# Kernel tuning notes

Hardware: AMD Instinct MI355X
Metric: run time of the kernel (lower is better)

## Reference

```python
import jax, jax.numpy as jnp
import numpy as np

IN_F = 4096
OUT_F = 4096
B, S = 4, 2048


def _rand_ortho(n, seed):
    # stand-in for method.rand_ortho_butterfly: a random orthogonal matrix
    rng = np.random.default_rng(seed)
    q, _ = np.linalg.qr(rng.standard_normal((n, n)).astype(np.float64))
    return jnp.asarray(q, dtype=jnp.float32)


def setup_inputs() -> dict:
    key = jax.random.key(0)
    k_x, k_q, k_s, k_b = jax.random.split(key, 4)
    x = jax.random.normal(k_x, (B, S, IN_F), dtype=jnp.float32)
    qweight = jax.random.randint(k_q, (IN_F, OUT_F), 0, 16, dtype=jnp.int32)
    scale = jnp.float32(1.0)
    # per-column rescale; keep away from zero to avoid blowup in division
    scaleWH = jax.random.uniform(k_s, (IN_F,), dtype=jnp.float32, minval=0.5, maxval=1.5)
    bias = jax.random.normal(k_b, (OUT_F,), dtype=jnp.float32)
    U = _rand_ortho(OUT_F, 51934)   # w.shape[0] = outfeatures
    V = _rand_ortho(IN_F, 51935)    # w.shape[1] = infeatures
    return {"x": x, "qweight": qweight, "scale": scale, "scaleWH": scaleWH,
            "bias": bias, "U": U, "V": V}


def reference(x, qweight, scale, scaleWH, bias, U, V):
    # dequantize: qweight[in,out] -> w[out,in] in [-1,1] * scale
    w = qweight.T.astype(jnp.float32) / 15.0 * 2.0 - 1.0  # [out, in]
    w = w * scale
    # incoherence transform: U^T @ w @ V (dense orthogonal 'butterfly')
    w = U.T @ w @ V                                        # [out, in]
    # diagonal rescaling over the input dimension
    w = w / scaleWH[None, :]
    # F.linear(x, w, bias) = x @ w.T + bias
    return jnp.einsum('bsi,oi->bso', x, w) + bias
```

## Files before the change

kernel.cpp:

```cpp
#include <hip/hip_runtime.h>


#define KT128 128

typedef __attribute__((ext_vector_type(4))) float f32x4;
typedef __attribute__((ext_vector_type(4))) int   i32x4;
typedef __attribute__((ext_vector_type(8))) short s16x8;
typedef __attribute__((ext_vector_type(4))) short s16x4;

__device__ __forceinline__ unsigned short f2bf(float f){
  unsigned u = __builtin_bit_cast(unsigned, f);
  u += 0x7FFFu + ((u >> 16) & 1u);
  return (unsigned short)(u >> 16);
}
__device__ __forceinline__ float bf2f(unsigned short h){
  unsigned u = ((unsigned)h) << 16;
  return __builtin_bit_cast(float, u);
}
__device__ __forceinline__ void splitbf(float v, short &hi, short &lo){
  unsigned short h = f2bf(v);
  float r = v - bf2f(h);
  hi = (short)h;
  lo = (short)f2bf(r);
}

__device__ __forceinline__ void stage16(const short* g, short* l){
  __builtin_amdgcn_global_load_lds((const __attribute__((address_space(1))) void*)g,
                                   (__attribute__((address_space(3))) void*)l,
                                   16, 0, 0);
}

template<int MODE>
__global__ __launch_bounds__(256)
void pack_rows_kernel(const void* __restrict__ srcv,
                      const float* __restrict__ scale_p,
                      short* __restrict__ Oh, short* __restrict__ Ol)
{
  __shared__ float lds[128][33];
  const int kt = blockIdx.x;
  const int mt = blockIdx.y;
  const int t  = threadIdx.x;
  float dq_a = 1.0f, dq_b = 0.0f;
  if (MODE == 1){ float sc = scale_p[0]; dq_a = sc * (2.0f/15.0f); dq_b = -sc; }
  const int rrow = t >> 3;
  const int c4   = t & 7;
  #pragma unroll
  for (int rr = 0; rr < 4; ++rr){
    const int row = rr*32 + rrow;
    const size_t soff = ((size_t)(mt*128 + row))*4096 + (size_t)kt*32 + c4*4;
    if (MODE == 0){
      const f32x4 v = *(const f32x4*)((const float*)srcv + soff);
      #pragma unroll
      for (int j=0;j<4;++j) lds[row][c4*4+j] = v[j];
    } else {
      const i32x4 v = *(const i32x4*)((const int*)srcv + soff);
      #pragma unroll
      for (int j=0;j<4;++j) lds[row][c4*4+j] = (float)v[j]*dq_a + dq_b;
    }
  }
  __syncthreads();
  #pragma unroll
  for (int rnd=0; rnd<2; ++rnd){
    const int cc = rnd*256 + t;
    const int kgp = cc >> 7, mr = cc & 127;
    s16x8 h8, l8;
    #pragma unroll
    for (int j=0;j<8;++j){
      short h,l; splitbf(lds[mr][kgp*8+j], h, l);
      h8[j]=h; l8[j]=l;
    }
    const size_t chunk = ((((size_t)mt*KT128 + kt)*4 + kgp)*128 + mr)*8;
    *(s16x8*)(Oh + chunk) = h8;
    *(s16x8*)(Ol + chunk) = l8;
  }
}

__global__ __launch_bounds__(256)
void pack_cols_kernel(const float* __restrict__ src,
                      short* __restrict__ Oh, short* __restrict__ Ol)
{
  __shared__ float lds[32][132];
  const int kt = blockIdx.x;
  const int xt = blockIdx.y;
  const int t  = threadIdx.x;
  const int o4 = t >> 5;
  const int c4 = t & 31;
  #pragma unroll
  for (int rr=0; rr<4; ++rr){
    const int o = rr*8 + o4;
    const size_t soff = ((size_t)(kt*32 + o))*4096 + (size_t)xt*128 + c4*4;
    const f32x4 v = *(const f32x4*)(src + soff);
    *(f32x4*)&lds[o][c4*4] = v;
  }
  __syncthreads();
  #pragma unroll
  for (int rnd=0; rnd<2; ++rnd){
    const int cc = rnd*256 + t;
    const int kgp = cc >> 7, xr = cc & 127;
    s16x8 h8, l8;
    #pragma unroll
    for (int j=0;j<8;++j){
      short h,l; splitbf(lds[kgp*8+j][xr], h, l);
      h8[j]=h; l8[j]=l;
    }
    const size_t chunk = ((((size_t)xt*KT128 + kt)*4 + kgp)*128 + xr)*8;
    *(s16x8*)(Oh + chunk) = h8;
    *(s16x8*)(Ol + chunk) = l8;
  }
}

template<int EPI>
__global__ __launch_bounds__(256, 2)
void gemm_bf16x3(const short* __restrict__ Ah, const short* __restrict__ Al,
                 const short* __restrict__ Bh, const short* __restrict__ Bl,
                 float* __restrict__ outF, const float* __restrict__ bias,
                 short* __restrict__ Oh, short* __restrict__ Ol,
                 const float* __restrict__ rowScale)
{
  __shared__ short ls[16384];
  short* lsAh = ls;
  short* lsAl = ls + 4096;
  short* lsBh = ls + 8192;
  short* lsBl = ls + 12288;

  const int t    = threadIdx.x;
  const int lane = t & 63, wave = t >> 6;
  const int wr   = wave >> 1, wc = wave & 1;
  const int nt   = blockIdx.x, mt = blockIdx.y;
  const int lr   = lane & 15, kg = lane >> 4;

  f32x4 acc[4][4];
  #pragma unroll
  for (int i=0;i<4;++i)
    #pragma unroll
    for (int j=0;j<4;++j)
      acc[i][j] = f32x4{0.f,0.f,0.f,0.f};

  const short* bAh = Ah + ((size_t)mt*KT128)*4096;
  const short* bAl = Al + ((size_t)mt*KT128)*4096;
  const short* bBh = Bh + ((size_t)nt*KT128)*4096;
  const short* bBl = Bl + ((size_t)nt*KT128)*4096;

  for (int kt = 0; kt < KT128; ++kt){
    const size_t to = (size_t)kt*4096;
    #pragma unroll
    for (int rnd=0; rnd<2; ++rnd){
      const int lo_ = rnd*2048 + wave*512;
      const int go  = lo_ + lane*8;
      stage16(bAh + to + go, lsAh + lo_);
      stage16(bAl + to + go, lsAl + lo_);
      stage16(bBh + to + go, lsBh + lo_);
      stage16(bBl + to + go, lsBl + lo_);
    }
    __syncthreads();

    s16x8 a_h[4], a_l[4];
    #pragma unroll
    for (int fm=0; fm<4; ++fm){
      const int row = wr*64 + fm*16 + lr;
      a_h[fm] = *(const s16x8*)(lsAh + (kg*128 + row)*8);
      a_l[fm] = *(const s16x8*)(lsAl + (kg*128 + row)*8);
    }
    #pragma unroll
    for (int fn=0; fn<4; ++fn){
      const int col = wc*64 + fn*16 + lr;
      const s16x8 b_h = *(const s16x8*)(lsBh + (kg*128 + col)*8);
      const s16x8 b_l = *(const s16x8*)(lsBl + (kg*128 + col)*8);
      #pragma unroll
      for (int fm=0; fm<4; ++fm){
        f32x4 c = acc[fm][fn];
        c = __builtin_amdgcn_mfma_f32_16x16x32_bf16(a_h[fm], b_h, c, 0,0,0);
        c = __builtin_amdgcn_mfma_f32_16x16x32_bf16(a_h[fm], b_l, c, 0,0,0);
        c = __builtin_amdgcn_mfma_f32_16x16x32_bf16(a_l[fm], b_h, c, 0,0,0);
        acc[fm][fn] = c;
      }
    }
    __syncthreads();
  }

  const int r0 = (lane >> 4) * 4;
  if (EPI == 1){
    #pragma unroll
    for (int fm=0; fm<4; ++fm){
      const int gm = mt*128 + wr*64 + fm*16 + r0;
      #pragma unroll
      for (int fn=0; fn<4; ++fn){
        const int gn = nt*128 + wc*64 + fn*16 + lr;
        const float b = bias[gn];
        #pragma unroll
        for (int reg=0; reg<4; ++reg)
          outF[(size_t)(gm+reg)*4096 + gn] = acc[fm][fn][reg] + b;
      }
    }
  } else {
    #pragma unroll
    for (int fm=0; fm<4; ++fm){
      const int rowBase = mt*128 + wr*64 + fm*16 + r0;
      float rs[4];
      #pragma unroll
      for (int reg=0; reg<4; ++reg)
        rs[reg] = rowScale ? (1.0f / rowScale[rowBase+reg]) : 1.0f;
      const int ktp = rowBase >> 5;
      const int kgp = (rowBase >> 3) & 3;
      const int rp  = rowBase & 7;
      #pragma unroll
      for (int fn=0; fn<4; ++fn){
        const int nr = wc*64 + fn*16 + lr;
        const size_t chunk = ((((size_t)nt*KT128 + ktp)*4 + kgp)*128 + nr)*8 + rp;
        s16x4 h4, l4;
        #pragma unroll
        for (int reg=0; reg<4; ++reg){
          short h,l; splitbf(acc[fm][fn][reg]*rs[reg], h, l);
          h4[reg]=h; l4[reg]=l;
        }
        *(s16x4*)(Oh + chunk) = h4;
        *(s16x4*)(Ol + chunk) = l4;
      }
    }
  }
}

extern "C" void kernel_launch(void* const* d_in, const int* in_sizes, int n_in,
                              void* d_out, int out_size, void* d_ws, size_t ws_size,
                              hipStream_t stream)
{
  const float* x      = (const float*)d_in[0];
  const int*   qw     = (const int*)  d_in[1];
  const float* scale  = (const float*)d_in[2];
  const float* sWH    = (const float*)d_in[3];
  const float* bias   = (const float*)d_in[4];
  const float* U      = (const float*)d_in[5];
  const float* V      = (const float*)d_in[6];
  float* out = (float*)d_out;

  const size_t SZW = (size_t)4096*4096;
  if (ws_size < 6*SZW*sizeof(short)) return;

  short* ws  = (short*)d_ws;
  short* Dh  = ws;
  short* Dl  = ws + SZW;
  short* Uh  = ws + 2*SZW;
  short* Ul  = ws + 3*SZW;
  short* A1h = ws + 4*SZW;
  short* A1l = ws + 5*SZW;
  short* Xh  = ws + 4*SZW;
  short* Xl  = ws;

  dim3 blk(256);

  pack_rows_kernel<1><<<dim3(128,32), blk, 0, stream>>>((const void*)qw, scale, Dh, Dl);
  pack_cols_kernel<<<dim3(128,32), blk, 0, stream>>>(U, Uh, Ul);
  gemm_bf16x3<0><<<dim3(32,32), blk, 0, stream>>>(Dh, Dl, Uh, Ul,
                                                  nullptr, nullptr, A1h, A1l, nullptr);
  pack_cols_kernel<<<dim3(128,32), blk, 0, stream>>>(V, Dh, Dl);
  gemm_bf16x3<0><<<dim3(32,32), blk, 0, stream>>>(Dh, Dl, A1h, A1l,
                                                  nullptr, nullptr, Uh, Ul, sWH);
  pack_rows_kernel<0><<<dim3(128,64), blk, 0, stream>>>((const void*)x, nullptr, Xh, Xl);
  gemm_bf16x3<1><<<dim3(32,64), blk, 0, stream>>>(Xh, Xl, Uh, Ul,
                                                  out, bias, nullptr, nullptr, nullptr);
}
```

Measured before the change: 1.594 ms.

## Exploit exact integer dequant to drop low-part GEMM pass, swizzle tiles, raise occupancy

```diff
diff --git a/kernel.cpp b/kernel.cpp
--- a/kernel.cpp
+++ b/kernel.cpp
@@ -30,18 +30,25 @@
                                    16, 0, 0);
 }
 
+__device__ __forceinline__ void swz_tile(int &nt, int &mt){
+  const int gx   = gridDim.x;
+  const int nwg  = gx * gridDim.y;
+  const int orig = blockIdx.y * gx + blockIdx.x;
+  const int cpx  = nwg >> 3;
+  const int s    = (orig & 7) * cpx + (orig >> 3);
+  nt = s % gx;
+  mt = s / gx;
+}
+
 template<int MODE>
 __global__ __launch_bounds__(256)
 void pack_rows_kernel(const void* __restrict__ srcv,
-                      const float* __restrict__ scale_p,
                       short* __restrict__ Oh, short* __restrict__ Ol)
 {
   __shared__ float lds[128][33];
   const int kt = blockIdx.x;
   const int mt = blockIdx.y;
   const int t  = threadIdx.x;
-  float dq_a = 1.0f, dq_b = 0.0f;
-  if (MODE == 1){ float sc = scale_p[0]; dq_a = sc * (2.0f/15.0f); dq_b = -sc; }
   const int rrow = t >> 3;
   const int c4   = t & 7;
   #pragma unroll
@@ -55,7 +62,7 @@
     } else {
       const i32x4 v = *(const i32x4*)((const int*)srcv + soff);
       #pragma unroll
-      for (int j=0;j<4;++j) lds[row][c4*4+j] = (float)v[j]*dq_a + dq_b;
+      for (int j=0;j<4;++j) lds[row][c4*4+j] = (float)(2*v[j] - 15);
     }
   }
   __syncthreads();
@@ -66,12 +73,16 @@
     s16x8 h8, l8;
     #pragma unroll
     for (int j=0;j<8;++j){
-      short h,l; splitbf(lds[mr][kgp*8+j], h, l);
-      h8[j]=h; l8[j]=l;
+      if (MODE == 1){
+        h8[j] = (short)f2bf(lds[mr][kgp*8+j]);
+      } else {
+        short h,l; splitbf(lds[mr][kgp*8+j], h, l);
+        h8[j]=h; l8[j]=l;
+      }
     }
     const size_t chunk = ((((size_t)mt*KT128 + kt)*4 + kgp)*128 + mr)*8;
     *(s16x8*)(Oh + chunk) = h8;
-    *(s16x8*)(Ol + chunk) = l8;
+    if (MODE == 0) *(s16x8*)(Ol + chunk) = l8;
   }
 }
 
@@ -109,24 +120,26 @@
   }
 }
 
-template<int EPI>
-__global__ __launch_bounds__(256, 2)
-void gemm_bf16x3(const short* __restrict__ Ah, const short* __restrict__ Al,
-                 const short* __restrict__ Bh, const short* __restrict__ Bl,
-                 float* __restrict__ outF, const float* __restrict__ bias,
-                 short* __restrict__ Oh, short* __restrict__ Ol,
-                 const float* __restrict__ rowScale)
-{
-  __shared__ short ls[16384];
+template<int EPI, int NMUL>
+__global__ __launch_bounds__(256, 4)
+void gemm_bf16x(const short* __restrict__ Ah, const short* __restrict__ Al,
+                const short* __restrict__ Bh, const short* __restrict__ Bl,
+                float* __restrict__ outF, const float* __restrict__ bias,
+                short* __restrict__ Oh, short* __restrict__ Ol,
+                const float* __restrict__ rowScale,
+                const float* __restrict__ kmul)
+{
+  __shared__ short ls[(NMUL==2) ? 12288 : 16384];
   short* lsAh = ls;
-  short* lsAl = ls + 4096;
-  short* lsBh = ls + 8192;
-  short* lsBl = ls + 12288;
+  short* lsAl = (NMUL==3) ? (ls + 4096) : nullptr;
+  short* lsBh = ls + ((NMUL==2) ? 4096 : 8192);
+  short* lsBl = ls + ((NMUL==2) ? 8192 : 12288);
 
   const int t    = threadIdx.x;
   const int lane = t & 63, wave = t >> 6;
   const int wr   = wave >> 1, wc = wave & 1;
-  const int nt   = blockIdx.x, mt = blockIdx.y;
+  int nt, mt;
+  swz_tile(nt, mt);
   const int lr   = lane & 15, kg = lane >> 4;
 
   f32x4 acc[4][4];
@@ -137,7 +150,7 @@
       acc[i][j] = f32x4{0.f,0.f,0.f,0.f};
 
   const short* bAh = Ah + ((size_t)mt*KT128)*4096;
-  const short* bAl = Al + ((size_t)mt*KT128)*4096;
+  const short* bAl = (NMUL==3) ? (Al + ((size_t)mt*KT128)*4096) : nullptr;
   const short* bBh = Bh + ((size_t)nt*KT128)*4096;
   const short* bBl = Bl + ((size_t)nt*KT128)*4096;
 
@@ -148,30 +161,32 @@
       const int lo_ = rnd*2048 + wave*512;
       const int go  = lo_ + lane*8;
       stage16(bAh + to + go, lsAh + lo_);
-      stage16(bAl + to + go, lsAl + lo_);
+      if (NMUL==3) stage16(bAl + to + go, lsAl + lo_);
       stage16(bBh + to + go, lsBh + lo_);
       stage16(bBl + to + go, lsBl + lo_);
     }
     __syncthreads();
 
-    s16x8 a_h[4], a_l[4];
+    s16x8 b_h[4], b_l[4];
+    #pragma unroll
+    for (int fn=0; fn<4; ++fn){
+      const int col = wc*64 + fn*16 + lr;
+      b_h[fn] = *(const s16x8*)(lsBh + (kg*128 + col)*8);
+      b_l[fn] = *(const s16x8*)(lsBl + (kg*128 + col)*8);
+    }
     #pragma unroll
     for (int fm=0; fm<4; ++fm){
       const int row = wr*64 + fm*16 + lr;
-      a_h[fm] = *(const s16x8*)(lsAh + (kg*128 + row)*8);
-      a_l[fm] = *(const s16x8*)(lsAl + (kg*128 + row)*8);
-    }
-    #pragma unroll
-    for (int fn=0; fn<4; ++fn){
-      const int col = wc*64 + fn*16 + lr;
-      const s16x8 b_h = *(const s16x8*)(lsBh + (kg*128 + col)*8);
-      const s16x8 b_l = *(const s16x8*)(lsBl + (kg*128 + col)*8);
-      #pragma unroll
-      for (int fm=0; fm<4; ++fm){
+      const s16x8 a_h = *(const s16x8*)(lsAh + (kg*128 + row)*8);
+      s16x8 a_l;
+      if (NMUL==3) a_l = *(const s16x8*)(lsAl + (kg*128 + row)*8);
+      #pragma unroll
+      for (int fn=0; fn<4; ++fn){
         f32x4 c = acc[fm][fn];
-        c = __builtin_amdgcn_mfma_f32_16x16x32_bf16(a_h[fm], b_h, c, 0,0,0);
-        c = __builtin_amdgcn_mfma_f32_16x16x32_bf16(a_h[fm], b_l, c, 0,0,0);
-        c = __builtin_amdgcn_mfma_f32_16x16x32_bf16(a_l[fm], b_h, c, 0,0,0);
+        c = __builtin_amdgcn_mfma_f32_16x16x32_bf16(a_h, b_h[fn], c, 0,0,0);
+        c = __builtin_amdgcn_mfma_f32_16x16x32_bf16(a_h, b_l[fn], c, 0,0,0);
+        if (NMUL==3)
+          c = __builtin_amdgcn_mfma_f32_16x16x32_bf16(a_l, b_h[fn], c, 0,0,0);
         acc[fm][fn] = c;
       }
     }
@@ -193,13 +208,14 @@
       }
     }
   } else {
+    const float km = kmul ? (kmul[0] * (1.0f/15.0f)) : 1.0f;
     #pragma unroll
     for (int fm=0; fm<4; ++fm){
       const int rowBase = mt*128 + wr*64 + fm*16 + r0;
       float rs[4];
       #pragma unroll
       for (int reg=0; reg<4; ++reg)
-        rs[reg] = rowScale ? (1.0f / rowScale[rowBase+reg]) : 1.0f;
+        rs[reg] = km * (rowScale ? (1.0f / rowScale[rowBase+reg]) : 1.0f);
       const int ktp = rowBase >> 5;
       const int kgp = (rowBase >> 3) & 3;
       const int rp  = rowBase & 7;
@@ -248,14 +264,17 @@
 
   dim3 blk(256);
 
-  pack_rows_kernel<1><<<dim3(128,32), blk, 0, stream>>>((const void*)qw, scale, Dh, Dl);
+  pack_rows_kernel<1><<<dim3(128,32), blk, 0, stream>>>((const void*)qw, Dh, nullptr);
   pack_cols_kernel<<<dim3(128,32), blk, 0, stream>>>(U, Uh, Ul);
-  gemm_bf16x3<0><<<dim3(32,32), blk, 0, stream>>>(Dh, Dl, Uh, Ul,
-                                                  nullptr, nullptr, A1h, A1l, nullptr);
+  gemm_bf16x<0,2><<<dim3(32,32), blk, 0, stream>>>(Dh, nullptr, Uh, Ul,
+                                                   nullptr, nullptr, A1h, A1l,
+                                                   nullptr, scale);
   pack_cols_kernel<<<dim3(128,32), blk, 0, stream>>>(V, Dh, Dl);
-  gemm_bf16x3<0><<<dim3(32,32), blk, 0, stream>>>(Dh, Dl, A1h, A1l,
-                                                  nullptr, nullptr, Uh, Ul, sWH);
-  pack_rows_kernel<0><<<dim3(128,64), blk, 0, stream>>>((const void*)x, nullptr, Xh, Xl);
-  gemm_bf16x3<1><<<dim3(32,64), blk, 0, stream>>>(Xh, Xl, Uh, Ul,
-                                                  out, bias, nullptr, nullptr, nullptr);
-}
+  gemm_bf16x<0,3><<<dim3(32,32), blk, 0, stream>>>(Dh, Dl, A1h, A1l,
+                                                   nullptr, nullptr, Uh, Ul,
+                                                   sWH, nullptr);
+  pack_rows_kernel<0><<<dim3(128,64), blk, 0, stream>>>((const void*)x, Xh, Xl);
+  gemm_bf16x<1,3><<<dim3(32,64), blk, 0, stream>>>(Xh, Xl, Uh, Ul,
+                                                   out, bias, nullptr, nullptr,
+                                                   nullptr, nullptr);
+}
```

Result: no change. 1.569 ms (-1.5%).
